# Performance work log

Measured on AMD Instinct MI355X. Metric: run time of the kernel, lower is better.

The kernel has to match this reference:

```python
import jax, jax.numpy as jnp
import numpy as np

B, H, W = 32768, 28, 28
HID = 800


def dft2(x):
    # centered 2D DFT: fftshift(fft2(ifftshift(x)))
    ax = (-2, -1)
    return jnp.fft.fftshift(jnp.fft.fft2(jnp.fft.ifftshift(x, axes=ax), axes=ax), axes=ax)


def idft2(x):
    ax = (-2, -1)
    return jnp.fft.fftshift(jnp.fft.ifft2(jnp.fft.ifftshift(x, axes=ax), axes=ax), axes=ax)


def setup_inputs() -> dict:
    key = jax.random.key(0)
    k = jax.random.split(key, 5)
    x = jax.random.normal(k[0], (B, H, W), dtype=jnp.float32)
    tmask_re = jnp.ones((1, H, W), dtype=jnp.float32)
    tmask_im = jnp.zeros((1, H, W), dtype=jnp.float32)
    w1 = jax.random.normal(k[1], (HID, H * W), dtype=jnp.float32) * 0.03
    b1 = jax.random.normal(k[2], (HID,), dtype=jnp.float32) * 0.03
    w4 = jax.random.normal(k[3], (10, HID), dtype=jnp.float32) * 0.03
    b4 = jax.random.normal(k[4], (10,), dtype=jnp.float32) * 0.03
    return {"x": x, "tmask_re": tmask_re, "tmask_im": tmask_im,
            "w1": w1, "b1": b1, "w4": w4, "b4": b4}


def reference(x, tmask_re, tmask_im, w1, b1, w4, b4):
    tmask = jax.lax.complex(tmask_re, tmask_im)          # [1,28,28] complex64
    xf = dft2(x.astype(jnp.complex64))                    # [B,28,28] complex64
    xf = tmask * xf                                       # elementwise complex mask
    xr = jnp.real(idft2(xf))                              # back to real image
    h = xr.reshape(-1, H * W)                             # [B,784]
    h = jax.nn.relu(h @ w1.T + b1)                        # [B,800]
    logits = h @ w4.T + b4                                # [B,10]
    return jax.nn.log_softmax(logits, axis=-1)
```

## Files before the change

### kernel.cpp

```cpp
#include <hip/hip_runtime.h>
#include <hip/hip_bf16.h>
#include <cmath>

typedef unsigned short u16;
typedef __attribute__((ext_vector_type(8))) short short8v;
typedef __attribute__((ext_vector_type(4))) unsigned short ushort4v;
typedef __attribute__((ext_vector_type(8))) unsigned short ushort8v;
typedef __attribute__((ext_vector_type(4))) float f32x4;

#define NPIX 784
#define KP   800
#define NH   800
#define STRIDE 808

__device__ __forceinline__ u16 f2bf(float f) {
    union { float f; unsigned int u; } v; v.f = f;
    unsigned int u = v.u;
    unsigned int r = (u + 0x7FFFu + ((u >> 16) & 1u)) >> 16;
    return (u16)r;
}

__global__ void k_kre(const float* __restrict__ MRE, const float* __restrict__ MIM,
                      float* __restrict__ KRE, float* __restrict__ FLAG)
{
    __shared__ float msre[784], msim[784], tre[784], tim[784];
    __shared__ float c28[28], s28[28];
    __shared__ int smax;

    const int t = threadIdx.x;
    if (t < 28) {
        float th = (float)t * (6.283185307179586f / 28.0f);
        s28[t] = sinf(th);
        c28[t] = cosf(th);
    }
    if (t == 0) smax = 0;
    if (t < 784) {
        int r = t / 28, c = t - r * 28;
        int idx = ((r + 14) % 28) * 28 + ((c + 14) % 28);
        msre[t] = MRE[idx];
        msim[t] = MIM[idx];
    }
    __syncthreads();
    if (t < 784) {
        int u = t / 28, cc = t - u * 28;
        float re = 0.f, im = 0.f;
        int ph = 0;
        for (int v = 0; v < 28; ++v) {
            float cr = c28[ph], ci = s28[ph];
            float ar = msre[u * 28 + v], ai = msim[u * 28 + v];
            re += ar * cr - ai * ci;
            im += ar * ci + ai * cr;
            ph += cc; if (ph >= 28) ph -= 28;
        }
        tre[t] = re; tim[t] = im;
    }
    __syncthreads();
    float dev = 0.f;
    if (t < 784) {
        int pr = t / 28, pc = t - pr * 28;
        float s = 0.f;
        int ph = 0;
        for (int u = 0; u < 28; ++u) {
            s += tre[u * 28 + pc] * c28[ph] - tim[u * 28 + pc] * s28[ph];
            ph += pr; if (ph >= 28) ph -= 28;
        }
        s *= (1.0f / 784.0f);
        KRE[t] = s;
        dev = fabsf(s - (t == 0 ? 1.0f : 0.0f));
    }
    #pragma unroll
    for (int m = 32; m >= 1; m >>= 1) dev = fmaxf(dev, __shfl_xor(dev, m, 64));
    if ((t & 63) == 0) atomicMax(&smax, __float_as_int(dev));
    __syncthreads();
    if (t == 0) FLAG[0] = (__int_as_float(smax) < 1e-4f) ? 1.0f : 0.0f;
}

__global__ void k_w1pack(const float* __restrict__ W1, const float* __restrict__ KRE,
                         const float* __restrict__ FLAG, u16* __restrict__ W1P)
{
    const int c = blockIdx.x;
    const int t = threadIdx.x;
    const bool delta = (FLAG[0] > 0.5f);
    __shared__ float w1d[56 * 56];
    __shared__ float kr[784];

    if (delta) {
        if (t < 100) {
            int k0 = t * 8;
            ushort8v h;
            if (k0 + 7 < NPIX) {
                const float4* wp = (const float4*)(W1 + (size_t)c * NPIX + k0);
                float4 a = wp[0], b = wp[1];
                h[0] = f2bf(a.x); h[1] = f2bf(a.y); h[2] = f2bf(a.z); h[3] = f2bf(a.w);
                h[4] = f2bf(b.x); h[5] = f2bf(b.y); h[6] = f2bf(b.z); h[7] = f2bf(b.w);
            } else {
                #pragma unroll
                for (int e = 0; e < 8; ++e) {
                    int k = k0 + e;
                    h[e] = (k < NPIX) ? f2bf(W1[(size_t)c * NPIX + k]) : (u16)0;
                }
            }
            int kf = k0 >> 5, r = k0 & 31;
            int l  = ((r >> 3) << 4) | (c & 15);
            int nf = c >> 4;
            ((ushort8v*)W1P)[(nf * 25 + kf) * 64 + l] = h;
        }
        return;
    }
    for (int i = t; i < 784; i += 128) kr[i] = KRE[i];
    for (int i = t; i < 3136; i += 128) {
        int r = i / 56, cc = i - r * 56;
        w1d[i] = W1[(size_t)c * NPIX + (r % 28) * 28 + (cc % 28)];
    }
    __syncthreads();
    for (int k = t; k < KP; k += 128) {
        float v = 0.f;
        if (k < NPIX) {
            int krr = k / 28, kcc = k - krr * 28;
            for (int dr = 0; dr < 28; ++dr) {
                const float* wrow = &w1d[(krr + dr) * 56 + kcc];
                const float* krow = &kr[dr * 28];
                #pragma unroll 4
                for (int dc = 0; dc < 28; ++dc) v += wrow[dc] * krow[dc];
            }
        }
        int kf = k >> 5, r = k & 31;
        int l  = ((r >> 3) << 4) | (c & 15);
        int nf = c >> 4;
        W1P[(size_t)(((nf * 25 + kf) * 64 + l) << 3) | (r & 7)] = f2bf(v);
    }
}

__global__ void k_w4pack(const float* __restrict__ W4, u16* __restrict__ W4P)
{
    int i = blockIdx.x * 256 + threadIdx.x;
    if (i >= 1600) return;
    int l = i & 63, kt = i >> 6;
    int lc = l & 15, lk = l >> 4;
    ushort8v h;
    #pragma unroll
    for (int e = 0; e < 8; ++e) {
        int k = kt * 32 + lk * 8 + e;
        h[e] = (lc < 10) ? f2bf(W4[lc * NH + k]) : (u16)0;
    }
    ((ushort8v*)W4P)[i] = h;
}

__global__ __launch_bounds__(640) __attribute__((amdgpu_waves_per_eu(3, 3)))
void k_main(
    const float* __restrict__ X, const u16* __restrict__ W1P,
    const u16* __restrict__ W4P, const float* __restrict__ B1,
    const float* __restrict__ B4, float* __restrict__ OUT)
{
    __shared__ __align__(16) u16 As[64 * STRIDE];
    __shared__ __align__(16) float PL2[10 * 4 * 64 * 4];

    const int t = threadIdx.x;
    const int row0 = blockIdx.x * 64;
    const int l = t & 63, w = t >> 6;
    const int lc = l & 15, lk = l >> 4;

    #pragma unroll
    for (int pass = 0; pass < 2; ++pass) {
        float4 y[10];
        #pragma unroll
        for (int i = 0; i < 10; ++i) {
            int idx = t + 640 * (pass * 10 + i);
            int row = idx / 200, q = idx - row * 200;
            if (q < 196)
                y[i] = *(const float4*)(X + (size_t)(row0 + row) * NPIX + (q << 2));
            else
                y[i] = make_float4(0.f, 0.f, 0.f, 0.f);
        }
        #pragma unroll
        for (int i = 0; i < 10; ++i) {
            int idx = t + 640 * (pass * 10 + i);
            int row = idx / 200, q = idx - row * 200;
            ushort4v h;
            h[0] = f2bf(y[i].x); h[1] = f2bf(y[i].y);
            h[2] = f2bf(y[i].z); h[3] = f2bf(y[i].w);
            *(ushort4v*)(As + row * STRIDE + (q << 2)) = h;
        }
    }

    f32x4 acc[4][5];
    #pragma unroll
    for (int m = 0; m < 4; ++m)
        #pragma unroll
        for (int n = 0; n < 5; ++n) acc[m][n] = (f32x4)(0.0f);

    const short8v* BP = (const short8v*)W1P;
    short8v bb[2][5];
    #pragma unroll
    for (int n = 0; n < 5; ++n)
        bb[0][n] = BP[((w * 5 + n) * 25 + 0) * 64 + l];

    __syncthreads();

    #pragma unroll
    for (int kt = 0; kt < 25; ++kt) {
        if (kt < 24) {
            #pragma unroll
            for (int n = 0; n < 5; ++n)
                bb[(kt + 1) & 1][n] = BP[((w * 5 + n) * 25 + (kt + 1)) * 64 + l];
        }
        const u16* ab = As + lc * STRIDE + kt * 32 + lk * 8;
        __builtin_amdgcn_s_setprio(1);
        #pragma unroll
        for (int m = 0; m < 4; ++m) {
            short8v a = *(const short8v*)(ab + m * (16 * STRIDE));
            #pragma unroll
            for (int n = 0; n < 5; ++n)
                acc[m][n] = __builtin_amdgcn_mfma_f32_16x16x32_bf16(a, bb[kt & 1][n], acc[m][n], 0, 0, 0);
        }
        __builtin_amdgcn_s_setprio(0);
    }
    __syncthreads();

    #pragma unroll
    for (int n = 0; n < 5; ++n) {
        float bn = B1[w * 80 + n * 16 + lc];
        #pragma unroll
        for (int m = 0; m < 4; ++m) {
            #pragma unroll
            for (int j = 0; j < 4; ++j) {
                float hv = fmaxf(acc[m][n][j] + bn, 0.0f);
                As[(m * 16 + lk * 4 + j) * STRIDE + (w * 80 + n * 16 + lc)] = f2bf(hv);
            }
        }
    }
    __syncthreads();

    {
        const int ks  = (w < 5) ? 3 * w : 15 + 2 * (w - 5);
        const int cnt = (w < 5) ? 3 : 2;
        const short8v* WP = (const short8v*)W4P;
        f32x4 pc[4];
        #pragma unroll
        for (int m = 0; m < 4; ++m) pc[m] = (f32x4)(0.0f);
        #pragma unroll
        for (int i = 0; i < 3; ++i) {
            if (i < cnt) {
                int kt = ks + i;
                short8v b = WP[kt * 64 + l];
                #pragma unroll
                for (int m = 0; m < 4; ++m) {
                    short8v a = *(const short8v*)(As + (m * 16 + lc) * STRIDE + kt * 32 + lk * 8);
                    pc[m] = __builtin_amdgcn_mfma_f32_16x16x32_bf16(a, b, pc[m], 0, 0, 0);
                }
            }
        }
        f32x4* PLv = (f32x4*)PL2;
        #pragma unroll
        for (int m = 0; m < 4; ++m)
            PLv[(w * 4 + m) * 64 + l] = pc[m];
    }
    __syncthreads();

    if (t < 64) {
        const int r = t;
        const int m = r >> 4, sub = ((r & 15) >> 2) * 16, j = r & 3;
        float lg[10];
        #pragma unroll
        for (int o = 0; o < 10; ++o) {
            float s = B4[o];
            #pragma unroll
            for (int w2 = 0; w2 < 10; ++w2)
                s += PL2[(((w2 * 4 + m) * 64) + sub + o) * 4 + j];
            lg[o] = s;
        }
        float mx = lg[0];
        #pragma unroll
        for (int o = 1; o < 10; ++o) mx = fmaxf(mx, lg[o]);
        float se = 0.f;
        #pragma unroll
        for (int o = 0; o < 10; ++o) se += expf(lg[o] - mx);
        float lse = logf(se);
        float* op = OUT + (size_t)(row0 + r) * 10;
        #pragma unroll
        for (int o = 0; o < 10; ++o) op[o] = lg[o] - mx - lse;
    }
}

extern "C" void kernel_launch(void* const* d_in, const int* in_sizes, int n_in,
                              void* d_out, int out_size, void* d_ws, size_t ws_size,
                              hipStream_t stream)
{
    const float* X   = (const float*)d_in[0];
    const float* MRE = (const float*)d_in[1];
    const float* MIM = (const float*)d_in[2];
    const float* W1  = (const float*)d_in[3];
    const float* B1  = (const float*)d_in[4];
    const float* W4  = (const float*)d_in[5];
    const float* B4  = (const float*)d_in[6];
    float* OUT = (float*)d_out;

    float* kre  = (float*)d_ws;
    float* flag = kre + 784;
    u16*   w1p  = (u16*)((char*)d_ws + 4096);
    u16*   w4p  = (u16*)((char*)d_ws + 4096 + 1310720);

    k_kre<<<1, 832, 0, stream>>>(MRE, MIM, kre, flag);
    k_w1pack<<<800, 128, 0, stream>>>(W1, kre, flag, w1p);
    k_w4pack<<<7, 256, 0, stream>>>(W4, w4p);
    k_main<<<512, 640, 0, stream>>>(X, w1p, w4p, B1, B4, OUT);
}
```

Baseline: 71.40 us.

## Split A-tile staging to overlap second half loads with first-half MFMAs

```diff
diff --git a/kernel.cpp b/kernel.cpp
--- a/kernel.cpp
+++ b/kernel.cpp
@@ -18,6 +18,15 @@
     unsigned int u = v.u;
     unsigned int r = (u + 0x7FFFu + ((u >> 16) & 1u)) >> 16;
     return (u16)r;
+}
+
+__device__ __forceinline__ ushort4v cvt4(float4 v) {
+    union { __hip_bfloat162 h; ushort2 u; } a, b;
+    a.h = __float22bfloat162_rn(make_float2(v.x, v.y));
+    b.h = __float22bfloat162_rn(make_float2(v.z, v.w));
+    ushort4v r;
+    r[0] = a.u.x; r[1] = a.u.y; r[2] = b.u.x; r[3] = b.u.y;
+    return r;
 }
 
 __global__ void k_kre(const float* __restrict__ MRE, const float* __restrict__ MIM,
@@ -161,25 +170,12 @@
     const int lc = l & 15, lk = l >> 4;
 
     #pragma unroll
-    for (int pass = 0; pass < 2; ++pass) {
-        float4 y[10];
-        #pragma unroll
-        for (int i = 0; i < 10; ++i) {
-            int idx = t + 640 * (pass * 10 + i);
-            int row = idx / 200, q = idx - row * 200;
-            if (q < 196)
-                y[i] = *(const float4*)(X + (size_t)(row0 + row) * NPIX + (q << 2));
-            else
-                y[i] = make_float4(0.f, 0.f, 0.f, 0.f);
-        }
-        #pragma unroll
-        for (int i = 0; i < 10; ++i) {
-            int idx = t + 640 * (pass * 10 + i);
-            int row = idx / 200, q = idx - row * 200;
-            ushort4v h;
-            h[0] = f2bf(y[i].x); h[1] = f2bf(y[i].y);
-            h[2] = f2bf(y[i].z); h[3] = f2bf(y[i].w);
-            *(ushort4v*)(As + row * STRIDE + (q << 2)) = h;
+    for (int ii = 0; ii < 11; ++ii) {
+        int idx = t + 640 * ii;
+        if (idx < 6656) {
+            int row = idx / 104, q = idx - row * 104;
+            float4 v = *(const float4*)(X + (size_t)(row0 + row) * NPIX + (q << 2));
+            *(ushort4v*)(As + row * STRIDE + (q << 2)) = cvt4(v);
         }
     }
 
@@ -198,7 +194,39 @@
     __syncthreads();
 
     #pragma unroll
-    for (int kt = 0; kt < 25; ++kt) {
+    for (int kt = 0; kt < 13; ++kt) {
+        #pragma unroll
+        for (int n = 0; n < 5; ++n)
+            bb[(kt + 1) & 1][n] = BP[((w * 5 + n) * 25 + (kt + 1)) * 64 + l];
+        if (kt < 10) {
+            int idx = t + 640 * kt;
+            if (idx < 6144) {
+                int row = idx / 96, q = idx - row * 96;
+                ushort4v h;
+                if (q < 92) {
+                    float4 v = *(const float4*)(X + (size_t)(row0 + row) * NPIX + 416 + (q << 2));
+                    h = cvt4(v);
+                } else {
+                    h[0] = 0; h[1] = 0; h[2] = 0; h[3] = 0;
+                }
+                *(ushort4v*)(As + row * STRIDE + 416 + (q << 2)) = h;
+            }
+        }
+        const u16* ab = As + lc * STRIDE + kt * 32 + lk * 8;
+        __builtin_amdgcn_s_setprio(1);
+        #pragma unroll
+        for (int m = 0; m < 4; ++m) {
+            short8v a = *(const short8v*)(ab + m * (16 * STRIDE));
+            #pragma unroll
+            for (int n = 0; n < 5; ++n)
+                acc[m][n] = __builtin_amdgcn_mfma_f32_16x16x32_bf16(a, bb[kt & 1][n], acc[m][n], 0, 0, 0);
+        }
+        __builtin_amdgcn_s_setprio(0);
+    }
+    __syncthreads();
+
+    #pragma unroll
+    for (int kt = 13; kt < 25; ++kt) {
         if (kt < 24) {
             #pragma unroll
             for (int n = 0; n < 5; ++n)
```

New measurement: 75.83 us. +6.2%, slower.

## Load X fragments directly from global into MFMA registers, skip LDS staging

Applied to the files above, without the earlier changes.

```diff
diff --git a/kernel.cpp b/kernel.cpp
--- a/kernel.cpp
+++ b/kernel.cpp
@@ -18,6 +18,18 @@
     unsigned int u = v.u;
     unsigned int r = (u + 0x7FFFu + ((u >> 16) & 1u)) >> 16;
     return (u16)r;
+}
+
+__device__ __forceinline__ short8v cvt8(float4 v0, float4 v1) {
+    union { __hip_bfloat162 h; ushort2 u; } a, b, c, d;
+    a.h = __float22bfloat162_rn(make_float2(v0.x, v0.y));
+    b.h = __float22bfloat162_rn(make_float2(v0.z, v0.w));
+    c.h = __float22bfloat162_rn(make_float2(v1.x, v1.y));
+    d.h = __float22bfloat162_rn(make_float2(v1.z, v1.w));
+    short8v r;
+    r[0] = (short)a.u.x; r[1] = (short)a.u.y; r[2] = (short)b.u.x; r[3] = (short)b.u.y;
+    r[4] = (short)c.u.x; r[5] = (short)c.u.y; r[6] = (short)d.u.x; r[7] = (short)d.u.y;
+    return r;
 }
 
 __global__ void k_kre(const float* __restrict__ MRE, const float* __restrict__ MIM,
@@ -160,29 +172,6 @@
     const int l = t & 63, w = t >> 6;
     const int lc = l & 15, lk = l >> 4;
 
-    #pragma unroll
-    for (int pass = 0; pass < 2; ++pass) {
-        float4 y[10];
-        #pragma unroll
-        for (int i = 0; i < 10; ++i) {
-            int idx = t + 640 * (pass * 10 + i);
-            int row = idx / 200, q = idx - row * 200;
-            if (q < 196)
-                y[i] = *(const float4*)(X + (size_t)(row0 + row) * NPIX + (q << 2));
-            else
-                y[i] = make_float4(0.f, 0.f, 0.f, 0.f);
-        }
-        #pragma unroll
-        for (int i = 0; i < 10; ++i) {
-            int idx = t + 640 * (pass * 10 + i);
-            int row = idx / 200, q = idx - row * 200;
-            ushort4v h;
-            h[0] = f2bf(y[i].x); h[1] = f2bf(y[i].y);
-            h[2] = f2bf(y[i].z); h[3] = f2bf(y[i].w);
-            *(ushort4v*)(As + row * STRIDE + (q << 2)) = h;
-        }
-    }
-
     f32x4 acc[4][5];
     #pragma unroll
     for (int m = 0; m < 4; ++m)
@@ -190,32 +179,52 @@
         for (int n = 0; n < 5; ++n) acc[m][n] = (f32x4)(0.0f);
 
     const short8v* BP = (const short8v*)W1P;
-    short8v bb[2][5];
-    #pragma unroll
-    for (int n = 0; n < 5; ++n)
-        bb[0][n] = BP[((w * 5 + n) * 25 + 0) * 64 + l];
-
-    __syncthreads();
+    const float* xb0 = X + (size_t)(row0 + lc) * NPIX + lk * 8;
+    const float* xb1 = xb0 + 16 * NPIX;
+    const float* xb2 = xb0 + 32 * NPIX;
+    const float* xb3 = xb0 + 48 * NPIX;
 
     #pragma unroll
     for (int kt = 0; kt < 25; ++kt) {
+        short8v b[5];
+        #pragma unroll
+        for (int n = 0; n < 5; ++n)
+            b[n] = BP[((w * 5 + n) * 25 + kt) * 64 + l];
+
+        short8v a[4];
         if (kt < 24) {
+            const float* p0 = xb0 + kt * 32;
+            const float* p1 = xb1 + kt * 32;
+            const float* p2 = xb2 + kt * 32;
+            const float* p3 = xb3 + kt * 32;
+            a[0] = cvt8(*(const float4*)(p0), *(const float4*)(p0 + 4));
+            a[1] = cvt8(*(const float4*)(p1), *(const float4*)(p1 + 4));
+            a[2] = cvt8(*(const float4*)(p2), *(const float4*)(p2 + 4));
+            a[3] = cvt8(*(const float4*)(p3), *(const float4*)(p3 + 4));
+        } else {
+            if (lk < 2) {
+                const float* p0 = xb0 + 24 * 32;
+                const float* p1 = xb1 + 24 * 32;
+                const float* p2 = xb2 + 24 * 32;
+                const float* p3 = xb3 + 24 * 32;
+                a[0] = cvt8(*(const float4*)(p0), *(const float4*)(p0 + 4));
+                a[1] = cvt8(*(const float4*)(p1), *(const float4*)(p1 + 4));
+                a[2] = cvt8(*(const float4*)(p2), *(const float4*)(p2 + 4));
+                a[3] = cvt8(*(const float4*)(p3), *(const float4*)(p3 + 4));
+            } else {
+                #pragma unroll
+                for (int m = 0; m < 4; ++m) a[m] = (short8v)(0);
+            }
+        }
+
+        __builtin_amdgcn_s_setprio(1);
+        #pragma unroll
+        for (int m = 0; m < 4; ++m)
             #pragma unroll
             for (int n = 0; n < 5; ++n)
-                bb[(kt + 1) & 1][n] = BP[((w * 5 + n) * 25 + (kt + 1)) * 64 + l];
-        }
-        const u16* ab = As + lc * STRIDE + kt * 32 + lk * 8;
-        __builtin_amdgcn_s_setprio(1);
-        #pragma unroll
-        for (int m = 0; m < 4; ++m) {
-            short8v a = *(const short8v*)(ab + m * (16 * STRIDE));
-            #pragma unroll
-            for (int n = 0; n < 5; ++n)
-                acc[m][n] = __builtin_amdgcn_mfma_f32_16x16x32_bf16(a, bb[kt & 1][n], acc[m][n], 0, 0, 0);
-        }
+                acc[m][n] = __builtin_amdgcn_mfma_f32_16x16x32_bf16(a[m], b[n], acc[m][n], 0, 0, 0);
         __builtin_amdgcn_s_setprio(0);
     }
-    __syncthreads();
 
     #pragma unroll
     for (int n = 0; n < 5; ++n) {
```

New measurement: 125.2 us. 1.75x slower.

## Stream X into LDS via async global_load_lds double buffering with in-loop bf16 conversion

Applied to the files above, without the earlier changes.

```diff
diff --git a/kernel.cpp b/kernel.cpp
--- a/kernel.cpp
+++ b/kernel.cpp
@@ -12,12 +12,33 @@
 #define KP   800
 #define NH   800
 #define STRIDE 808
+#define CHB  40960
+#define ROWB 640
 
 __device__ __forceinline__ u16 f2bf(float f) {
     union { float f; unsigned int u; } v; v.f = f;
     unsigned int u = v.u;
     unsigned int r = (u + 0x7FFFu + ((u >> 16) & 1u)) >> 16;
     return (u16)r;
+}
+
+__device__ __forceinline__ short8v cvt8(f32x4 v0, f32x4 v1) {
+    union { __hip_bfloat162 h; ushort2 u; } a, b, c, d;
+    a.h = __float22bfloat162_rn(make_float2(v0[0], v0[1]));
+    b.h = __float22bfloat162_rn(make_float2(v0[2], v0[3]));
+    c.h = __float22bfloat162_rn(make_float2(v1[0], v1[1]));
+    d.h = __float22bfloat162_rn(make_float2(v1[2], v1[3]));
+    short8v r;
+    r[0] = (short)a.u.x; r[1] = (short)a.u.y; r[2] = (short)b.u.x; r[3] = (short)b.u.y;
+    r[4] = (short)c.u.x; r[5] = (short)c.u.y; r[6] = (short)d.u.x; r[7] = (short)d.u.y;
+    return r;
+}
+
+__device__ __forceinline__ void gload16(const float* g, void* l) {
+    __builtin_amdgcn_global_load_lds(
+        (const __attribute__((address_space(1))) unsigned int*)g,
+        (__attribute__((address_space(3))) unsigned int*)l,
+        16, 0, 0);
 }
 
 __global__ void k_kre(const float* __restrict__ MRE, const float* __restrict__ MIM,
@@ -152,36 +173,32 @@
     const u16* __restrict__ W4P, const float* __restrict__ B1,
     const float* __restrict__ B4, float* __restrict__ OUT)
 {
-    __shared__ __align__(16) u16 As[64 * STRIDE];
-    __shared__ __align__(16) float PL2[10 * 4 * 64 * 4];
+    __shared__ __align__(16) char SMEM[144384];
+    char*  xb0 = SMEM;
+    char*  xb1 = SMEM + CHB;
+    u16*   As  = (u16*)SMEM;
+    float* PL2 = (float*)(SMEM + 103424);
 
     const int t = threadIdx.x;
     const int row0 = blockIdx.x * 64;
     const int l = t & 63, w = t >> 6;
     const int lc = l & 15, lk = l >> 4;
 
-    #pragma unroll
-    for (int pass = 0; pass < 2; ++pass) {
-        float4 y[10];
-        #pragma unroll
-        for (int i = 0; i < 10; ++i) {
-            int idx = t + 640 * (pass * 10 + i);
-            int row = idx / 200, q = idx - row * 200;
-            if (q < 196)
-                y[i] = *(const float4*)(X + (size_t)(row0 + row) * NPIX + (q << 2));
-            else
-                y[i] = make_float4(0.f, 0.f, 0.f, 0.f);
-        }
-        #pragma unroll
-        for (int i = 0; i < 10; ++i) {
-            int idx = t + 640 * (pass * 10 + i);
-            int row = idx / 200, q = idx - row * 200;
-            ushort4v h;
-            h[0] = f2bf(y[i].x); h[1] = f2bf(y[i].y);
-            h[2] = f2bf(y[i].z); h[3] = f2bf(y[i].w);
-            *(ushort4v*)(As + row * STRIDE + (q << 2)) = h;
-        }
-    }
+    const int r0s  = t / 40;
+    const int cs16 = (t - r0s * 40) * 16;
+    const int swzS = (r0s & 7) << 4;
+    const int colb = cs16 ^ swzS;
+    const bool ok4 = colb < 576;
+    const float* gp[4];
+    #pragma unroll
+    for (int i = 0; i < 4; ++i)
+        gp[i] = X + (size_t)(row0 + r0s + 16 * i) * NPIX + (colb >> 2);
+    const int lb = 16 * t;
+
+    const int swzA = (lc & 7) << 4;
+    const int q0 = (lk * 32) ^ swzA;
+    const int q1 = q0 ^ 16;
+    const int arow = lc * ROWB;
 
     f32x4 acc[4][5];
     #pragma unroll
@@ -194,26 +211,58 @@
     #pragma unroll
     for (int n = 0; n < 5; ++n)
         bb[0][n] = BP[((w * 5 + n) * 25 + 0) * 64 + l];
-
-    __syncthreads();
-
-    #pragma unroll
-    for (int kt = 0; kt < 25; ++kt) {
-        if (kt < 24) {
+    __builtin_amdgcn_sched_barrier(0);
+
+    #pragma unroll
+    for (int i = 0; i < 4; ++i) gload16(gp[i], xb0 + lb + i * 10240);
+    #pragma unroll
+    for (int i = 0; i < 4; ++i) gload16(gp[i] + 160, xb1 + lb + i * 10240);
+    asm volatile("s_waitcnt vmcnt(4)" ::: "memory");
+    __builtin_amdgcn_s_barrier();
+    __builtin_amdgcn_sched_barrier(0);
+
+    #pragma unroll
+    for (int c = 0; c < 5; ++c) {
+        const char* bufc = (c & 1) ? xb1 : xb0;
+        #pragma unroll
+        for (int kf = 0; kf < 5; ++kf) {
+            const int kt = c * 5 + kf;
+            if (kt < 24) {
+                #pragma unroll
+                for (int n = 0; n < 5; ++n)
+                    bb[(kt + 1) & 1][n] = BP[((w * 5 + n) * 25 + (kt + 1)) * 64 + l];
+            }
+            const char* ab = bufc + arow + kf * 128;
+            __builtin_amdgcn_s_setprio(1);
             #pragma unroll
-            for (int n = 0; n < 5; ++n)
-                bb[(kt + 1) & 1][n] = BP[((w * 5 + n) * 25 + (kt + 1)) * 64 + l];
-        }
-        const u16* ab = As + lc * STRIDE + kt * 32 + lk * 8;
-        __builtin_amdgcn_s_setprio(1);
-        #pragma unroll
-        for (int m = 0; m < 4; ++m) {
-            short8v a = *(const short8v*)(ab + m * (16 * STRIDE));
-            #pragma unroll
-            for (int n = 0; n < 5; ++n)
-                acc[m][n] = __builtin_amdgcn_mfma_f32_16x16x32_bf16(a, bb[kt & 1][n], acc[m][n], 0, 0, 0);
-        }
-        __builtin_amdgcn_s_setprio(0);
+            for (int m = 0; m < 4; ++m) {
+                f32x4 v0 = *(const f32x4*)(ab + m * 10240 + q0);
+                f32x4 v1 = *(const f32x4*)(ab + m * 10240 + q1);
+                short8v a = cvt8(v0, v1);
+                #pragma unroll
+                for (int n = 0; n < 5; ++n)
+                    acc[m][n] = __builtin_amdgcn_mfma_f32_16x16x32_bf16(a, bb[kt & 1][n], acc[m][n], 0, 0, 0);
+            }
+            __builtin_amdgcn_s_setprio(0);
+        }
+        if (c < 4) {
+            __builtin_amdgcn_sched_barrier(0);
+            __builtin_amdgcn_s_barrier();
+            if (c < 3) {
+                char* dst = (c & 1) ? xb1 : xb0;
+                const int ch = c + 2;
+                #pragma unroll
+                for (int i = 0; i < 4; ++i) {
+                    const float* g = (ch == 4 && !ok4) ? X : gp[i] + ch * 160;
+                    gload16(g, dst + lb + i * 10240);
+                }
+                asm volatile("s_waitcnt vmcnt(4)" ::: "memory");
+            } else {
+                asm volatile("s_waitcnt vmcnt(5)" ::: "memory");
+            }
+            __builtin_amdgcn_s_barrier();
+            __builtin_amdgcn_sched_barrier(0);
+        }
     }
     __syncthreads();
 
```

New measurement: 72.27 us. No clear change (+1.2%).
